# Kernel tuning notes

Hardware: AMD Instinct MI355X
Metric: run time of the kernel (lower is better)

Reference implementation:

```python
import jax, jax.numpy as jnp
import numpy as np

NUM_EXPERTS = 8
TOP_K = 2
DIM = 1024
HIDDEN = 4096
B, S = 4, 2048


def setup_inputs() -> dict:
    key = jax.random.key(0)
    ks = jax.random.split(key, 6)
    scale = 0.02
    x = jax.random.normal(ks[0], (B, S, DIM), dtype=jnp.float32)
    wg = jax.random.normal(ks[1], (NUM_EXPERTS, DIM), dtype=jnp.float32) * scale
    bg = jnp.zeros((NUM_EXPERTS,), dtype=jnp.float32)
    Wgate = jax.random.normal(ks[2], (NUM_EXPERTS, HIDDEN, DIM), dtype=jnp.float32) * scale
    Wup = jax.random.normal(ks[3], (NUM_EXPERTS, HIDDEN, DIM), dtype=jnp.float32) * scale
    Wdown = jax.random.normal(ks[4], (NUM_EXPERTS, DIM, HIDDEN), dtype=jnp.float32) * scale
    return {"x": x, "wg": wg, "bg": bg, "Wgate": Wgate, "Wup": Wup, "Wdown": Wdown}


def reference(x, wg, bg, Wgate, Wup, Wdown):
    b, s, d = x.shape
    xf = x.reshape(-1, d)  # [T, D]
    T = xf.shape[0]
    # --- gating: top-k over router logits, softmax over masked logits ---
    logits = xf @ wg.T + bg  # [T, E]
    vals, idx = jax.lax.top_k(logits, TOP_K)  # [T, K]
    masked = jnp.full_like(logits, -jnp.inf)
    rows = jnp.arange(T)[:, None]
    masked = masked.at[rows, idx].set(vals)
    weights = jax.nn.softmax(masked, axis=-1)  # zeros outside top-k
    # --- experts: weighted SwiGLU sum (weight is 0 for non-routed tokens,
    # so this matches the gather/scatter loop exactly) ---
    out = jnp.zeros_like(xf)
    for e in range(NUM_EXPERTS):
        g = xf @ Wgate[e].T            # [T, H]
        u = xf @ Wup[e].T              # [T, H]
        h = (g * jax.nn.sigmoid(g)) * u
        out = out + (h @ Wdown[e].T) * weights[:, e:e + 1]
    return out.reshape(b, s, d)
```

## Files before the change

kernel.cpp:

```cpp
#include <hip/hip_runtime.h>
#include <cstdint>
#include <cstddef>

typedef unsigned short ushort_t;
typedef __attribute__((ext_vector_type(8))) __bf16 bf16x8;
typedef __attribute__((ext_vector_type(8))) short  s16x8;
typedef __attribute__((ext_vector_type(4))) float  f32x4;

#define NE 8
#define DIM 1024
#define HIDDEN 4096
#define NTOK 8192
#define CAP NTOK
#define NROWS (NTOK * 2)

#define BM 128
#define BN 64
#define BN2 128
#define BK 32
#define LDP 40

static constexpr size_t WS_COUNTS  = 0;
static constexpr size_t WS_OFFSETS = 256;
static constexpr size_t WS_TPAIR   = 512;
static constexpr size_t WS_TOKENS  = WS_TPAIR + (size_t)NTOK * 2 * 4;
static constexpr size_t WS_WEIGHTS = WS_TOKENS + (size_t)NE * CAP * 4;
static constexpr size_t WS_H       = ((WS_WEIGHTS + (size_t)NE * CAP * 4 + 1023) / 1024) * 1024;
static constexpr size_t H_BYTES    = (size_t)NROWS * HIDDEN * 2;
static constexpr size_t WS_XB      = WS_H + H_BYTES;
static constexpr size_t XB_BYTES   = (size_t)NTOK * DIM * 2;
static constexpr size_t W_BYTES    = (size_t)NE * HIDDEN * DIM * 2;
static constexpr size_t WS_WA      = WS_XB + XB_BYTES;
static constexpr size_t WS_WUB     = WS_WA + W_BYTES;
static constexpr size_t WS_Y       = WS_WUB;
static constexpr size_t WS_T1_END  = WS_WUB + W_BYTES;

__device__ __forceinline__ ushort_t cvt_bf16(float f) {
  unsigned u = __float_as_uint(f);
  return (ushort_t)((u + 0x7FFFu + ((u >> 16) & 1u)) >> 16);
}

__device__ __forceinline__ void st8(ushort_t* dst, float4 a, float4 b) {
  s16x8 v;
  v[0] = (short)cvt_bf16(a.x); v[1] = (short)cvt_bf16(a.y);
  v[2] = (short)cvt_bf16(a.z); v[3] = (short)cvt_bf16(a.w);
  v[4] = (short)cvt_bf16(b.x); v[5] = (short)cvt_bf16(b.y);
  v[6] = (short)cvt_bf16(b.z); v[7] = (short)cvt_bf16(b.w);
  *reinterpret_cast<s16x8*>(dst) = v;
}

__device__ __forceinline__ bf16x8 ldb(const ushort_t* p) {
  union { s16x8 s; bf16x8 b; } u;
  u.s = *reinterpret_cast<const s16x8*>(p);
  return u.b;
}

__device__ __forceinline__ bf16x8 ldt(const ushort_t* base, int row, int s) {
  return ldb(base + (size_t)((row << 2) + (s ^ ((row >> 1) & 3))) * 8);
}

__device__ __forceinline__ f32x4 mfma16(bf16x8 a, bf16x8 b, f32x4 c) {
  return __builtin_amdgcn_mfma_f32_16x16x32_bf16(a, b, c, 0, 0, 0);
}

#define GLDS16(g, l)                                                     \
  __builtin_amdgcn_global_load_lds(                                      \
      (const __attribute__((address_space(1))) unsigned int*)(g),        \
      (__attribute__((address_space(3))) unsigned int*)(l), 16, 0, 0)

__global__ __launch_bounds__(256) void cvt_kernel(const float* __restrict__ s,
                                                  ushort_t* __restrict__ d, long n8) {
  long i = (long)blockIdx.x * 256 + threadIdx.x;
  long stride = (long)gridDim.x * 256;
  for (long p = i; p < n8; p += stride) {
    const float4* sp = reinterpret_cast<const float4*>(s) + 2 * p;
    float4 a = sp[0];
    float4 b = sp[1];
    st8(d + p * 8, a, b);
  }
}

__global__ __launch_bounds__(256) void cvt3_kernel(
    const float* __restrict__ s0, ushort_t* __restrict__ d0, long n0,
    const float* __restrict__ s1, ushort_t* __restrict__ d1, long n1,
    const float* __restrict__ s2, ushort_t* __restrict__ d2, long n2) {
  long i = (long)blockIdx.x * 256 + threadIdx.x;
  long stride = (long)gridDim.x * 256;
  long ntot = n0 + n1 + n2;
  for (long p = i; p < ntot; p += stride) {
    const float* s; ushort_t* d; long q = p;
    if (q < n0)            { s = s0; d = d0; }
    else if ((q -= n0) < n1) { s = s1; d = d1; }
    else                   { q -= n1; s = s2; d = d2; }
    const float4* sp = reinterpret_cast<const float4*>(s) + 2 * q;
    float4 a = sp[0];
    float4 b = sp[1];
    st8(d + q * 8, a, b);
  }
}

__global__ __launch_bounds__(256) void gating_kernel(
    const float* __restrict__ x, const float* __restrict__ wg,
    const float* __restrict__ bg, int* __restrict__ counts,
    int* __restrict__ token_list, float* __restrict__ weight_list,
    int* __restrict__ tpair) {
  int gid  = blockIdx.x * blockDim.x + threadIdx.x;
  int tok  = gid >> 6;
  int lane = threadIdx.x & 63;
  if (tok >= NTOK) return;
  const float* xr = x + (size_t)tok * DIM;

  float part[NE];
#pragma unroll
  for (int e = 0; e < NE; ++e) part[e] = 0.f;
  for (int i = lane; i < DIM; i += 64) {
    float xv = xr[i];
#pragma unroll
    for (int e = 0; e < NE; ++e) part[e] = fmaf(xv, wg[e * DIM + i], part[e]);
  }
#pragma unroll
  for (int e = 0; e < NE; ++e) {
    float v = part[e];
#pragma unroll
    for (int o = 32; o > 0; o >>= 1) v += __shfl_xor(v, o, 64);
    part[e] = v + bg[e];
  }
  if (lane == 0) {
    int i0 = 0; float v0 = part[0];
#pragma unroll
    for (int e = 1; e < NE; ++e) if (part[e] > v0) { v0 = part[e]; i0 = e; }
    int i1 = -1; float v1 = -INFINITY;
#pragma unroll
    for (int e = 0; e < NE; ++e) if (e != i0 && part[e] > v1) { v1 = part[e]; i1 = e; }
    float e1 = expf(v1 - v0);
    float s  = 1.f + e1;
    float w0 = 1.f / s;
    float w1 = e1 / s;
    int s0 = atomicAdd(&counts[i0], 1);
    token_list[i0 * CAP + s0]  = tok;
    weight_list[i0 * CAP + s0] = w0;
    tpair[tok * 2 + 0] = i0 * CAP + s0;
    int s1 = atomicAdd(&counts[i1], 1);
    token_list[i1 * CAP + s1]  = tok;
    weight_list[i1 * CAP + s1] = w1;
    tpair[tok * 2 + 1] = i1 * CAP + s1;
  }
}

__global__ void prefix_kernel(const int* __restrict__ counts, int* __restrict__ offsets) {
  if (threadIdx.x == 0) {
    int acc = 0;
    for (int e = 0; e < NE; ++e) { offsets[e] = acc; acc += counts[e]; }
  }
}

__global__ __launch_bounds__(256) void stage1_kernel(
    const ushort_t* __restrict__ xb, const ushort_t* __restrict__ wgb,
    const ushort_t* __restrict__ wub, const int* __restrict__ counts,
    const int* __restrict__ offsets, const int* __restrict__ token_list,
    ushort_t* __restrict__ h) {
  const int e  = blockIdx.z;
  const int mt = blockIdx.y;
  const int nt = blockIdx.x;
  const int count = counts[e];
  if (mt * BM >= count) return;

  __shared__ __align__(16) ushort_t XsL[BM * 32];
  __shared__ __align__(16) ushort_t GsL[BN * 32];
  __shared__ __align__(16) ushort_t UsL[BN * 32];
  __shared__ int toks[BM];

  const int t = threadIdx.x;
  if (t < BM) {
    int m = mt * BM + t;
    toks[t] = token_list[e * CAP + (m < count ? m : count - 1)];
  }
  __syncthreads();

  const int wid  = t >> 6;
  const int lane = t & 63;
  const int wm   = wid & 1;
  const int wn   = wid >> 1;
  const int fr   = lane & 15;
  const int kg   = lane >> 4;

  const int uA = wid * 128 + lane;
  const int uB = uA + 64;
  const int rA = uA >> 2, sA = (uA & 3) ^ ((rA >> 1) & 3);
  const int rB = uB >> 2, sB = (uB & 3) ^ ((rB >> 1) & 3);
  const ushort_t* gxA = xb + (size_t)toks[rA] * DIM + sA * 8;
  const ushort_t* gxB = xb + (size_t)toks[rB] * DIM + sB * 8;

  const int uG = wid * 64 + lane;
  const int rG = uG >> 2, sG = (uG & 3) ^ ((rG >> 1) & 3);
  const size_t wrow = (size_t)e * HIDDEN + (size_t)nt * BN + rG;
  const ushort_t* ggp = wgb + wrow * DIM + sG * 8;
  const ushort_t* gup = wub + wrow * DIM + sG * 8;

  ushort_t* ldsXA = XsL + (size_t)(wid * 128) * 8;
  ushort_t* ldsXB = XsL + (size_t)(wid * 128 + 64) * 8;
  ushort_t* ldsG  = GsL + (size_t)(wid * 64) * 8;
  ushort_t* ldsU  = UsL + (size_t)(wid * 64) * 8;

  f32x4 accg[4][2], accu[4][2];
#pragma unroll
  for (int i = 0; i < 4; ++i)
#pragma unroll
    for (int j = 0; j < 2; ++j) { accg[i][j] = (f32x4)0.f; accu[i][j] = (f32x4)0.f; }

  for (int k0 = 0; k0 < DIM; k0 += BK) {
    GLDS16(gxA + k0, ldsXA);
    GLDS16(gxB + k0, ldsXB);
    GLDS16(ggp + k0, ldsG);
    GLDS16(gup + k0, ldsU);
    __syncthreads();

    bf16x8 bg0 = ldt(GsL, wn * 32 + fr, kg);
    bf16x8 bg1 = ldt(GsL, wn * 32 + 16 + fr, kg);
    bf16x8 bu0 = ldt(UsL, wn * 32 + fr, kg);
    bf16x8 bu1 = ldt(UsL, wn * 32 + 16 + fr, kg);
#pragma unroll
    for (int mf = 0; mf < 4; ++mf) {
      bf16x8 a = ldt(XsL, wm * 64 + mf * 16 + fr, kg);
      accg[mf][0] = mfma16(a, bg0, accg[mf][0]);
      accg[mf][1] = mfma16(a, bg1, accg[mf][1]);
      accu[mf][0] = mfma16(a, bu0, accu[mf][0]);
      accu[mf][1] = mfma16(a, bu1, accu[mf][1]);
    }
    __syncthreads();
  }

  const size_t slot0 = (size_t)offsets[e];
  const int nbase = nt * BN + wn * 32;
#pragma unroll
  for (int mf = 0; mf < 4; ++mf) {
#pragma unroll
    for (int r = 0; r < 4; ++r) {
      int ml = wm * 64 + mf * 16 + kg * 4 + r;
      int m  = mt * BM + ml;
      if (m < count) {
        size_t rowoff = (slot0 + m) * (size_t)HIDDEN + nbase;
#pragma unroll
        for (int nf = 0; nf < 2; ++nf) {
          float g  = accg[mf][nf][r];
          float uu = accu[mf][nf][r];
          float hv = g / (1.f + __expf(-g)) * uu;
          h[rowoff + nf * 16 + fr] = cvt_bf16(hv);
        }
      }
    }
  }
}

__global__ __launch_bounds__(256) void stage2_y_kernel(
    const ushort_t* __restrict__ h, const ushort_t* __restrict__ wdb,
    const int* __restrict__ counts, const int* __restrict__ offsets,
    float* __restrict__ y) {
  const int e  = blockIdx.z;
  const int mt = blockIdx.y;
  const int nt = blockIdx.x;
  const int count = counts[e];
  if (mt * BM >= count) return;

  __shared__ __align__(16) ushort_t AsL[BM * 32];
  __shared__ __align__(16) ushort_t DsL[BN2 * 32];

  const int t = threadIdx.x;
  const int wid  = t >> 6;
  const int lane = t & 63;
  const int wm   = wid & 1;
  const int wn   = wid >> 1;
  const int fr   = lane & 15;
  const int kg   = lane >> 4;

  const int slot0b = offsets[e] + mt * BM;

  const int uA = wid * 128 + lane;
  const int uB = uA + 64;
  const int rA = uA >> 2, sA = (uA & 3) ^ ((rA >> 1) & 3);
  const int rB = uB >> 2, sB = (uB & 3) ^ ((rB >> 1) & 3);
  int hrA = slot0b + rA; hrA = hrA < NROWS ? hrA : NROWS - 1;
  int hrB = slot0b + rB; hrB = hrB < NROWS ? hrB : NROWS - 1;
  const ushort_t* ghA = h + (size_t)hrA * HIDDEN + sA * 8;
  const ushort_t* ghB = h + (size_t)hrB * HIDDEN + sB * 8;

  const ushort_t* gdA = wdb + ((size_t)e * DIM + (size_t)nt * BN2 + rA) * HIDDEN + sA * 8;
  const ushort_t* gdB = wdb + ((size_t)e * DIM + (size_t)nt * BN2 + rB) * HIDDEN + sB * 8;

  ushort_t* ldsAA = AsL + (size_t)(wid * 128) * 8;
  ushort_t* ldsAB = AsL + (size_t)(wid * 128 + 64) * 8;
  ushort_t* ldsDA = DsL + (size_t)(wid * 128) * 8;
  ushort_t* ldsDB = DsL + (size_t)(wid * 128 + 64) * 8;

  f32x4 acc[4][4];
#pragma unroll
  for (int i = 0; i < 4; ++i)
#pragma unroll
    for (int j = 0; j < 4; ++j) acc[i][j] = (f32x4)0.f;

  for (int k0 = 0; k0 < HIDDEN; k0 += BK) {
    GLDS16(ghA + k0, ldsAA);
    GLDS16(ghB + k0, ldsAB);
    GLDS16(gdA + k0, ldsDA);
    GLDS16(gdB + k0, ldsDB);
    __syncthreads();

    bf16x8 b[4];
#pragma unroll
    for (int nf = 0; nf < 4; ++nf) b[nf] = ldt(DsL, wn * 64 + nf * 16 + fr, kg);
#pragma unroll
    for (int mf = 0; mf < 4; ++mf) {
      bf16x8 a = ldt(AsL, wm * 64 + mf * 16 + fr, kg);
#pragma unroll
      for (int nf = 0; nf < 4; ++nf) acc[mf][nf] = mfma16(a, b[nf], acc[mf][nf]);
    }
    __syncthreads();
  }

  const int nbase = nt * BN2 + wn * 64;
#pragma unroll
  for (int mf = 0; mf < 4; ++mf) {
#pragma unroll
    for (int r = 0; r < 4; ++r) {
      int ml = wm * 64 + mf * 16 + kg * 4 + r;
      int m  = mt * BM + ml;
      if (m < count) {
        size_t row = (size_t)(slot0b + ml);
#pragma unroll
        for (int nf = 0; nf < 4; ++nf) {
          y[row * DIM + nbase + nf * 16 + fr] = acc[mf][nf][r];
        }
      }
    }
  }
}

__global__ __launch_bounds__(256) void combine_kernel(
    const float* __restrict__ y, const int* __restrict__ tpair,
    const float* __restrict__ weight_list, const int* __restrict__ offsets,
    float* __restrict__ out) {
  const int tok = blockIdx.x;
  const int v0 = tpair[tok * 2 + 0];
  const int v1 = tpair[tok * 2 + 1];
  const float w0 = weight_list[v0];
  const float w1 = weight_list[v1];
  const int s0 = offsets[v0 >> 13] + (v0 & (CAP - 1));
  const int s1 = offsets[v1 >> 13] + (v1 & (CAP - 1));
  const int d = threadIdx.x * 4;
  float4 a = *reinterpret_cast<const float4*>(y + (size_t)s0 * DIM + d);
  float4 b = *reinterpret_cast<const float4*>(y + (size_t)s1 * DIM + d);
  float4 o;
  o.x = w0 * a.x + w1 * b.x;
  o.y = w0 * a.y + w1 * b.y;
  o.z = w0 * a.z + w1 * b.z;
  o.w = w0 * a.w + w1 * b.w;
  *reinterpret_cast<float4*>(out + (size_t)tok * DIM + d) = o;
}

__global__ __launch_bounds__(256) void stage1_f32w(
    const float* __restrict__ x, const float* __restrict__ Wgate,
    const float* __restrict__ Wup, const int* __restrict__ counts,
    const int* __restrict__ offsets, const int* __restrict__ token_list,
    ushort_t* __restrict__ h) {
  const int e  = blockIdx.z;
  const int mt = blockIdx.y;
  const int nt = blockIdx.x;
  const int count = counts[e];
  if (mt * BM >= count) return;

  __shared__ __align__(16) ushort_t Xs[BM][LDP];
  __shared__ __align__(16) ushort_t Gs[BN][LDP];
  __shared__ __align__(16) ushort_t Us[BN][LDP];
  __shared__ int toks[BM];

  const int t = threadIdx.x;
  if (t < BM) {
    int m = mt * BM + t;
    toks[t] = token_list[e * CAP + (m < count ? m : count - 1)];
  }
  __syncthreads();

  const float* Wg = Wgate + (size_t)e * HIDDEN * DIM + (size_t)(nt * BN) * DIM;
  const float* Wu = Wup   + (size_t)e * HIDDEN * DIM + (size_t)(nt * BN) * DIM;

  const int wid  = t >> 6;
  const int lane = t & 63;
  const int wm   = wid & 1;
  const int wn   = wid >> 1;
  const int fr   = lane & 15;
  const int kg   = lane >> 4;

  f32x4 accg[4][2], accu[4][2];
#pragma unroll
  for (int i = 0; i < 4; ++i)
#pragma unroll
    for (int j = 0; j < 2; ++j) { accg[i][j] = (f32x4)0.f; accu[i][j] = (f32x4)0.f; }

  const int sr = t >> 2;
  const int sc = (t & 3) * 8;

  const int tok0 = toks[sr];
  const int tok1 = toks[sr + 64];
  const float* xp0 = x + (size_t)tok0 * DIM + sc;
  const float* xp1 = x + (size_t)tok1 * DIM + sc;
  const float* gp  = Wg + (size_t)sr * DIM + sc;
  const float* up  = Wu + (size_t)sr * DIM + sc;

  for (int k0 = 0; k0 < DIM; k0 += BK) {
    float4 a0 = *reinterpret_cast<const float4*>(xp0 + k0);
    float4 a1 = *reinterpret_cast<const float4*>(xp0 + k0 + 4);
    float4 b0 = *reinterpret_cast<const float4*>(xp1 + k0);
    float4 b1 = *reinterpret_cast<const float4*>(xp1 + k0 + 4);
    float4 g0 = *reinterpret_cast<const float4*>(gp + k0);
    float4 g1 = *reinterpret_cast<const float4*>(gp + k0 + 4);
    float4 u0 = *reinterpret_cast<const float4*>(up + k0);
    float4 u1 = *reinterpret_cast<const float4*>(up + k0 + 4);
    st8(&Xs[sr][sc],      a0, a1);
    st8(&Xs[sr + 64][sc], b0, b1);
    st8(&Gs[sr][sc],      g0, g1);
    st8(&Us[sr][sc],      u0, u1);
    __syncthreads();

    bf16x8 bg0 = ldb(&Gs[wn * 32 + fr][kg * 8]);
    bf16x8 bg1 = ldb(&Gs[wn * 32 + 16 + fr][kg * 8]);
    bf16x8 bu0 = ldb(&Us[wn * 32 + fr][kg * 8]);
    bf16x8 bu1 = ldb(&Us[wn * 32 + 16 + fr][kg * 8]);
#pragma unroll
    for (int mf = 0; mf < 4; ++mf) {
      bf16x8 a = ldb(&Xs[wm * 64 + mf * 16 + fr][kg * 8]);
      accg[mf][0] = mfma16(a, bg0, accg[mf][0]);
      accg[mf][1] = mfma16(a, bg1, accg[mf][1]);
      accu[mf][0] = mfma16(a, bu0, accu[mf][0]);
      accu[mf][1] = mfma16(a, bu1, accu[mf][1]);
    }
    __syncthreads();
  }

  const size_t slot0 = (size_t)offsets[e];
  const int nbase = nt * BN + wn * 32;
#pragma unroll
  for (int mf = 0; mf < 4; ++mf) {
#pragma unroll
    for (int r = 0; r < 4; ++r) {
      int ml = wm * 64 + mf * 16 + kg * 4 + r;
      int m  = mt * BM + ml;
      if (m < count) {
        size_t rowoff = (slot0 + m) * (size_t)HIDDEN + nbase;
#pragma unroll
        for (int nf = 0; nf < 2; ++nf) {
          float g  = accg[mf][nf][r];
          float uu = accu[mf][nf][r];
          float hv = g / (1.f + __expf(-g)) * uu;
          h[rowoff + nf * 16 + fr] = cvt_bf16(hv);
        }
      }
    }
  }
}

__global__ __launch_bounds__(256) void stage2_f32w(
    const ushort_t* __restrict__ h, const float* __restrict__ Wdown,
    const int* __restrict__ counts, const int* __restrict__ offsets,
    const int* __restrict__ token_list, const float* __restrict__ weight_list,
    float* __restrict__ out) {
  const int e  = blockIdx.z;
  const int mt = blockIdx.y;
  const int nt = blockIdx.x;
  const int count = counts[e];
  if (mt * BM >= count) return;

  __shared__ __align__(16) ushort_t As[BM][LDP];
  __shared__ __align__(16) ushort_t Ds[BN][LDP];
  __shared__ int   toks[BM];
  __shared__ float wts[BM];

  const int t = threadIdx.x;
  if (t < BM) {
    int m  = mt * BM + t;
    int mc = m < count ? m : count - 1;
    toks[t] = token_list[e * CAP + mc];
    wts[t]  = weight_list[e * CAP + mc];
  }
  __syncthreads();

  const float* Wd = Wdown + (size_t)e * DIM * HIDDEN + (size_t)(nt * BN) * HIDDEN;
  const int slot0b = offsets[e] + mt * BM;

  const int wid  = t >> 6;
  const int lane = t & 63;
  const int wm   = wid & 1;
  const int wn   = wid >> 1;
  const int fr   = lane & 15;
  const int kg   = lane >> 4;

  f32x4 acc[4][2];
#pragma unroll
  for (int i = 0; i < 4; ++i)
#pragma unroll
    for (int j = 0; j < 2; ++j) acc[i][j] = (f32x4)0.f;

  const int sr = t >> 2;
  const int sc = (t & 3) * 8;

  int r0 = slot0b + sr;       r0 = r0 < NROWS ? r0 : NROWS - 1;
  int r1 = slot0b + sr + 64;  r1 = r1 < NROWS ? r1 : NROWS - 1;
  const ushort_t* hp0 = h + (size_t)r0 * HIDDEN + sc;
  const ushort_t* hp1 = h + (size_t)r1 * HIDDEN + sc;
  const float*    dp  = Wd + (size_t)sr * HIDDEN + sc;

  for (int k0 = 0; k0 < HIDDEN; k0 += BK) {
    s16x8 ha = *reinterpret_cast<const s16x8*>(hp0 + k0);
    s16x8 hb = *reinterpret_cast<const s16x8*>(hp1 + k0);
    float4 d0 = *reinterpret_cast<const float4*>(dp + k0);
    float4 d1 = *reinterpret_cast<const float4*>(dp + k0 + 4);
    *reinterpret_cast<s16x8*>(&As[sr][sc])      = ha;
    *reinterpret_cast<s16x8*>(&As[sr + 64][sc]) = hb;
    st8(&Ds[sr][sc], d0, d1);
    __syncthreads();

    bf16x8 b0 = ldb(&Ds[wn * 32 + fr][kg * 8]);
    bf16x8 b1 = ldb(&Ds[wn * 32 + 16 + fr][kg * 8]);
#pragma unroll
    for (int mf = 0; mf < 4; ++mf) {
      bf16x8 a = ldb(&As[wm * 64 + mf * 16 + fr][kg * 8]);
      acc[mf][0] = mfma16(a, b0, acc[mf][0]);
      acc[mf][1] = mfma16(a, b1, acc[mf][1]);
    }
    __syncthreads();
  }

  const int nbase = nt * BN + wn * 32;
#pragma unroll
  for (int mf = 0; mf < 4; ++mf) {
#pragma unroll
    for (int r = 0; r < 4; ++r) {
      int ml = wm * 64 + mf * 16 + kg * 4 + r;
      int m  = mt * BM + ml;
      if (m < count) {
        int   tok = toks[ml];
        float w   = wts[ml];
        size_t o  = (size_t)tok * DIM + nbase;
#pragma unroll
        for (int nf = 0; nf < 2; ++nf) {
          atomicAdd(&out[o + nf * 16 + fr], acc[mf][nf][r] * w);
        }
      }
    }
  }
}

extern "C" void kernel_launch(void* const* d_in, const int* in_sizes, int n_in,
                              void* d_out, int out_size, void* d_ws, size_t ws_size,
                              hipStream_t stream) {
  const float* x     = (const float*)d_in[0];
  const float* wg    = (const float*)d_in[1];
  const float* bg    = (const float*)d_in[2];
  const float* Wgate = (const float*)d_in[3];
  const float* Wup   = (const float*)d_in[4];
  const float* Wdown = (const float*)d_in[5];
  float* out = (float*)d_out;

  char* ws = (char*)d_ws;
  int*      counts      = (int*)(ws + WS_COUNTS);
  int*      offsets     = (int*)(ws + WS_OFFSETS);
  int*      tpair       = (int*)(ws + WS_TPAIR);
  int*      token_list  = (int*)(ws + WS_TOKENS);
  float*    weight_list = (float*)(ws + WS_WEIGHTS);
  ushort_t* h           = (ushort_t*)(ws + WS_H);

  hipMemsetAsync(counts, 0, NE * sizeof(int), stream);

  gating_kernel<<<NTOK / 4, 256, 0, stream>>>(x, wg, bg, counts, token_list,
                                              weight_list, tpair);
  prefix_kernel<<<1, 64, 0, stream>>>(counts, offsets);

  if (ws_size >= WS_T1_END) {
    ushort_t* xb  = (ushort_t*)(ws + WS_XB);
    ushort_t* wA  = (ushort_t*)(ws + WS_WA);
    ushort_t* wub = (ushort_t*)(ws + WS_WUB);
    float*    y   = (float*)(ws + WS_Y);

    long w8 = (long)NE * HIDDEN * DIM / 8;
    long x8 = (long)NTOK * DIM / 8;
    cvt3_kernel<<<8192, 256, 0, stream>>>(Wgate, wA, w8, Wup, wub, w8, x, xb, x8);

    stage1_kernel<<<dim3(HIDDEN / BN, CAP / BM, NE), 256, 0, stream>>>(
        xb, wA, wub, counts, offsets, token_list, h);

    cvt_kernel<<<8192, 256, 0, stream>>>(Wdown, wA, w8);

    stage2_y_kernel<<<dim3(DIM / BN2, CAP / BM, NE), 256, 0, stream>>>(
        h, wA, counts, offsets, y);
    combine_kernel<<<NTOK, 256, 0, stream>>>(y, tpair, weight_list, offsets, out);
  } else {
    hipMemsetAsync(out, 0, (size_t)NTOK * DIM * sizeof(float), stream);
    stage1_f32w<<<dim3(HIDDEN / BN, CAP / BM, NE), 256, 0, stream>>>(
        x, Wgate, Wup, counts, offsets, token_list, h);
    stage2_f32w<<<dim3(DIM / BN, CAP / BM, NE), 256, 0, stream>>>(
        h, Wdown, counts, offsets, token_list, weight_list, out);
  }
}
```

Measured before the change: 1.244 ms.

## Fuse x bf16 conversion into gating and remap GEMM grids for XCD locality

The gating kernel now also converts its block's four token rows of x to bf16, so the cvt3 kernel no longer reads x a second time. The stage1 and stage2 GEMMs switch to a flat 1D grid with a remapping that places consecutive workgroups of the same expert and M-tile on one XCD (blockIdx mod 8). This is meant to improve L2 reuse of weight and activation tiles across the chiplets. In the fallback path the gating kernel writes its bf16 copy of x into the h buffer, which stage1_f32w later overwrites, so that conversion is wasted work there.

```diff
diff --git a/kernel.cpp b/kernel.cpp
--- a/kernel.cpp
+++ b/kernel.cpp
@@ -103,7 +103,7 @@
     const float* __restrict__ x, const float* __restrict__ wg,
     const float* __restrict__ bg, int* __restrict__ counts,
     int* __restrict__ token_list, float* __restrict__ weight_list,
-    int* __restrict__ tpair) {
+    int* __restrict__ tpair, ushort_t* __restrict__ xb) {
   int gid  = blockIdx.x * blockDim.x + threadIdx.x;
   int tok  = gid >> 6;
   int lane = threadIdx.x & 63;
@@ -145,6 +145,16 @@
     weight_list[i1 * CAP + s1] = w1;
     tpair[tok * 2 + 1] = i1 * CAP + s1;
   }
+
+  const size_t xoff = (size_t)blockIdx.x * 4 * DIM;
+#pragma unroll
+  for (int g = 0; g < 2; ++g) {
+    int u = threadIdx.x + g * 256;
+    const float4* sp = reinterpret_cast<const float4*>(x + xoff) + 2 * u;
+    float4 a = sp[0];
+    float4 b = sp[1];
+    st8(xb + xoff + (size_t)u * 8, a, b);
+  }
 }
 
 __global__ void prefix_kernel(const int* __restrict__ counts, int* __restrict__ offsets) {
@@ -159,9 +169,11 @@
     const ushort_t* __restrict__ wub, const int* __restrict__ counts,
     const int* __restrict__ offsets, const int* __restrict__ token_list,
     ushort_t* __restrict__ h) {
-  const int e  = blockIdx.z;
-  const int mt = blockIdx.y;
-  const int nt = blockIdx.x;
+  constexpr int NWG = (HIDDEN / BN) * (CAP / BM) * NE;
+  int id = ((int)blockIdx.x & 7) * (NWG / 8) + ((int)blockIdx.x >> 3);
+  const int nt = id & 63;
+  const int mt = (id >> 6) & 63;
+  const int e  = id >> 12;
   const int count = counts[e];
   if (mt * BM >= count) return;
 
@@ -256,9 +268,11 @@
     const ushort_t* __restrict__ h, const ushort_t* __restrict__ wdb,
     const int* __restrict__ counts, const int* __restrict__ offsets,
     float* __restrict__ y) {
-  const int e  = blockIdx.z;
-  const int mt = blockIdx.y;
-  const int nt = blockIdx.x;
+  constexpr int NWG = (DIM / BN2) * (CAP / BM) * NE;
+  int id = ((int)blockIdx.x & 7) * (NWG / 8) + ((int)blockIdx.x >> 3);
+  const int nt = id & 7;
+  const int mt = (id >> 3) & 63;
+  const int e  = id >> 9;
   const int count = counts[e];
   if (mt * BM >= count) return;
 
@@ -570,10 +584,6 @@
 
   hipMemsetAsync(counts, 0, NE * sizeof(int), stream);
 
-  gating_kernel<<<NTOK / 4, 256, 0, stream>>>(x, wg, bg, counts, token_list,
-                                              weight_list, tpair);
-  prefix_kernel<<<1, 64, 0, stream>>>(counts, offsets);
-
   if (ws_size >= WS_T1_END) {
     ushort_t* xb  = (ushort_t*)(ws + WS_XB);
     ushort_t* wA  = (ushort_t*)(ws + WS_WA);
@@ -581,18 +591,26 @@
     float*    y   = (float*)(ws + WS_Y);
 
     long w8 = (long)NE * HIDDEN * DIM / 8;
-    long x8 = (long)NTOK * DIM / 8;
-    cvt3_kernel<<<8192, 256, 0, stream>>>(Wgate, wA, w8, Wup, wub, w8, x, xb, x8);
-
-    stage1_kernel<<<dim3(HIDDEN / BN, CAP / BM, NE), 256, 0, stream>>>(
+
+    gating_kernel<<<NTOK / 4, 256, 0, stream>>>(x, wg, bg, counts, token_list,
+                                                weight_list, tpair, xb);
+    prefix_kernel<<<1, 64, 0, stream>>>(counts, offsets);
+
+    cvt3_kernel<<<8192, 256, 0, stream>>>(Wgate, wA, w8, Wup, wub, w8,
+                                          nullptr, nullptr, 0);
+
+    stage1_kernel<<<(HIDDEN / BN) * (CAP / BM) * NE, 256, 0, stream>>>(
         xb, wA, wub, counts, offsets, token_list, h);
 
     cvt_kernel<<<8192, 256, 0, stream>>>(Wdown, wA, w8);
 
-    stage2_y_kernel<<<dim3(DIM / BN2, CAP / BM, NE), 256, 0, stream>>>(
+    stage2_y_kernel<<<(DIM / BN2) * (CAP / BM) * NE, 256, 0, stream>>>(
         h, wA, counts, offsets, y);
     combine_kernel<<<NTOK, 256, 0, stream>>>(y, tpair, weight_list, offsets, out);
   } else {
+    gating_kernel<<<NTOK / 4, 256, 0, stream>>>(x, wg, bg, counts, token_list,
+                                                weight_list, tpair, h );
+    prefix_kernel<<<1, 64, 0, stream>>>(counts, offsets);
     hipMemsetAsync(out, 0, (size_t)NTOK * DIM * sizeof(float), stream);
     stage1_f32w<<<dim3(HIDDEN / BN, CAP / BM, NE), 256, 0, stream>>>(
         x, Wgate, Wup, counts, offsets, token_list, h);
```

After: 1.311 ms. 1.05x slower.
